# Kernel optimization log

Measured on AMD Instinct MI355X. Metric: run time of the kernel, lower is better.

Reference implementation:

```python
import jax, jax.numpy as jnp
import numpy as np

N_SRC0, N_DST0 = 100000, 20000   # block0: 100k src -> 20k dst
N_DST1 = 4096                    # block1: 20k src -> 4096 dst (seed nodes)


def setup_inputs() -> dict:
    key = jax.random.key(0)
    ks = jax.random.split(key, 8)
    E0, E1 = 640000, 131072
    return {
        "features": jax.random.normal(ks[0], (N_SRC0, 256), jnp.float32),
        "W1": jax.random.normal(ks[1], (256, 256), jnp.float32) * (1.0 / np.sqrt(256)),
        "b1": jnp.zeros((256,), jnp.float32),
        "W2": jax.random.normal(ks[2], (256, 128), jnp.float32) * (1.0 / np.sqrt(256)),
        "b2": jnp.zeros((128,), jnp.float32),
        "src0": jax.random.randint(ks[3], (E0,), 0, N_SRC0, jnp.int32),
        "dst0": jax.random.randint(ks[4], (E0,), 0, N_DST0, jnp.int32),
        "src1": jax.random.randint(ks[5], (E1,), 0, N_DST0, jnp.int32),
        "dst1": jax.random.randint(ks[6], (E1,), 0, N_DST1, jnp.int32),
    }


def _graph_conv(src, dst, n_dst, feat, W, b):
    # DGL GraphConv, norm='both': D_out^{-1/2} gather-sum D_in^{-1/2}, then WX+b.
    n_src = feat.shape[0]
    ones = jnp.ones(src.shape[0], feat.dtype)
    out_deg = jax.ops.segment_sum(ones, src, num_segments=n_src)
    norm_src = jnp.clip(out_deg, 1.0, None) ** -0.5          # [n_src]
    h = feat * norm_src[:, None]
    agg = jax.ops.segment_sum(h[src], dst, num_segments=n_dst)  # sparse SpMM
    in_deg = jax.ops.segment_sum(ones, dst, num_segments=n_dst)
    norm_dst = jnp.clip(in_deg, 1.0, None) ** -0.5           # [n_dst]
    return (agg * norm_dst[:, None]) @ W + b


def reference(features, W1, b1, W2, b2, src0, dst0, src1, dst1):
    x = jax.nn.relu(_graph_conv(src0, dst0, N_DST0, features, W1, b1))
    x = _graph_conv(src1, dst1, N_DST1, x, W2, b2)
    return x
```

## Files before the change

### kernel.cpp

```cpp
#include <hip/hip_runtime.h>
#include <hip/hip_bf16.h>

#define K_DIM 256
#define RSTRIDE 128
#define EPB 8192

#define G0_DB 625
#define G0_SB 256
#define G0_SW 392
#define G0_DCAP 48
#define G0_SCAP 80
#define G1_DB 128
#define G1_SB 64
#define G1_SW 313
#define G1_DCAP 128
#define G1_SCAP 224

typedef short bf16x8 __attribute__((ext_vector_type(8)));
typedef float f32x4 __attribute__((ext_vector_type(4)));

static __device__ __forceinline__ unsigned short f2bf(float x) {
    __hip_bfloat16 b = __float2bfloat16(x);
    return *reinterpret_cast<unsigned short*>(&b);
}
static __device__ __forceinline__ float bflo(unsigned int p) {
    return __uint_as_float(p << 16);
}
static __device__ __forceinline__ float bfhi(unsigned int p) {
    return __uint_as_float(p & 0xffff0000u);
}

template <int NDB, int NSB, int SW, int DCAP, int SCP>
static __device__ __forceinline__ void split_graph_sp(
        const int* __restrict__ src, const int* __restrict__ dst, int E, int chunk,
        int* __restrict__ gdcnt, int* __restrict__ gscnt,
        unsigned int* __restrict__ bdst, unsigned int* __restrict__ bsrc,
        int* sh) {
    const int tid = threadIdx.x;
    const int e0 = chunk * EPB;
    const int n = min(EPB, E - e0);
    for (int i = tid; i < NDB + NSB; i += 256) sh[i] = 0;
    __syncthreads();
    for (int j = tid; j < n; j += 256) {
        int d = dst[e0 + j];
        int s = src[e0 + j];
        int bD = d >> 5;
        int rD = atomicAdd(&sh[bD], 1);
        if (rD < DCAP) bdst[((size_t)chunk * NDB + bD) * DCAP + rD] =
            ((unsigned)s << 5) | (unsigned)(d & 31);
        int bS = (int)((unsigned)s / SW);
        int rS = atomicAdd(&sh[NDB + bS], 1);
        if (rS < SCP) bsrc[((size_t)chunk * NSB + bS) * SCP + rS] = (unsigned)s;
    }
    __syncthreads();
    for (int i = tid; i < NDB; i += 256) gdcnt[chunk * NDB + i] = min(sh[i], DCAP);
    for (int i = tid; i < NSB; i += 256) gscnt[chunk * NSB + i] = min(sh[NDB + i], SCP);
}

__global__ __launch_bounds__(256) void split_mega_kernel(
        const int* __restrict__ src0, const int* __restrict__ dst0, int E0,
        const int* __restrict__ src1, const int* __restrict__ dst1, int E1,
        int* __restrict__ gdcnt0, int* __restrict__ gscnt0,
        unsigned int* __restrict__ bdst0, unsigned int* __restrict__ bsrc0,
        int* __restrict__ gdcnt1, int* __restrict__ gscnt1,
        unsigned int* __restrict__ bdst1, unsigned int* __restrict__ bsrc1,
        int nA0, int nA1,
        const float* __restrict__ feat, unsigned short* __restrict__ h, int total_f,
        int castBlocks,
        const float* __restrict__ W1, uint4* __restrict__ pw1,
        const float* __restrict__ W2, uint4* __restrict__ pw2) {
    __shared__ int sh[G0_DB + G0_SB];
    const int b = blockIdx.x;
    if (b < nA0) {
        split_graph_sp<G0_DB, G0_SB, G0_SW, G0_DCAP, G0_SCAP>(
            src0, dst0, E0, b, gdcnt0, gscnt0, bdst0, bsrc0, sh);
    } else if (b < nA0 + nA1) {
        split_graph_sp<G1_DB, G1_SB, G1_SW, G1_DCAP, G1_SCAP>(
            src1, dst1, E1, b - nA0, gdcnt1, gscnt1, bdst1, bsrc1, sh);
    } else if (b < nA0 + nA1 + castBlocks) {
        int idx = ((b - nA0 - nA1) * blockDim.x + threadIdx.x) * 8;
        if (idx >= total_f) return;
        const float4 v0 = *reinterpret_cast<const float4*>(feat + idx);
        const float4 v1 = *reinterpret_cast<const float4*>(feat + idx + 4);
        union { ushort4 u4[2]; uint4 u; } o;
        o.u4[0].x = f2bf(v0.x); o.u4[0].y = f2bf(v0.y);
        o.u4[0].z = f2bf(v0.z); o.u4[0].w = f2bf(v0.w);
        o.u4[1].x = f2bf(v1.x); o.u4[1].y = f2bf(v1.y);
        o.u4[1].z = f2bf(v1.z); o.u4[1].w = f2bf(v1.w);
        *reinterpret_cast<uint4*>(h + idx) = o.u;
    } else if (b < nA0 + nA1 + castBlocks + 32) {
        int idx = (b - nA0 - nA1 - castBlocks) * blockDim.x + threadIdx.x;
        int lane = idx & 63;
        int kt = (idx >> 6) & 7;
        int nt = idx >> 9;
        int n = nt * 16 + (lane & 15);
        int k = kt * 32 + (lane >> 4) * 8;
        union { unsigned short us[8]; uint4 u; } o;
#pragma unroll
        for (int j = 0; j < 8; ++j) o.us[j] = f2bf(W1[(size_t)(k + j) * 256 + n]);
        pw1[idx] = o.u;
    } else {
        int idx = (b - nA0 - nA1 - castBlocks - 32) * blockDim.x + threadIdx.x;
        int lane = idx & 63;
        int kt = (idx >> 6) & 7;
        int nt = idx >> 9;
        int n = nt * 16 + (lane & 15);
        int k = kt * 32 + (lane >> 4) * 8;
        union { unsigned short us[8]; uint4 u; } o;
#pragma unroll
        for (int j = 0; j < 8; ++j) o.us[j] = f2bf(W2[(size_t)(k + j) * 128 + n]);
        pw2[idx] = o.u;
    }
}

__global__ __launch_bounds__(256) void finalize_kernel(
        int nA0, int nA1,
        const unsigned int* __restrict__ bdst0, const int* __restrict__ gdcnt0,
        int* __restrict__ cnt0, int* __restrict__ esrc0,
        const unsigned int* __restrict__ bdst1, const int* __restrict__ gdcnt1,
        int* __restrict__ cnt1, int* __restrict__ esrc1,
        const unsigned int* __restrict__ bsrc0, const int* __restrict__ gscnt0,
        int* __restrict__ od0,
        const unsigned int* __restrict__ bsrc1, const int* __restrict__ gscnt1,
        int* __restrict__ od1) {
    __shared__ int sh[G0_SW];
    const int tid = threadIdx.x;
    int b = blockIdx.x;
    if (b < G0_DB + G1_DB) {
        const bool g0 = b < G0_DB;
        if (!g0) b -= G0_DB;
        const unsigned int* __restrict__ bd = g0 ? bdst0 : bdst1;
        const int* __restrict__ gc = g0 ? gdcnt0 : gdcnt1;
        const int NDB = g0 ? G0_DB : G1_DB;
        const int DCAP = g0 ? G0_DCAP : G1_DCAP;
        const int nblk = g0 ? nA0 : nA1;
        int* __restrict__ esrc = g0 ? esrc0 : esrc1;
        int* __restrict__ cnt = g0 ? cnt0 : cnt1;
        if (tid < 32) sh[tid] = 0;
        __syncthreads();
        for (int rr = (tid >> 2); rr < nblk; rr += 64) {
            const int c = gc[rr * NDB + b];
            const unsigned int* __restrict__ seg = bd + ((size_t)rr * NDB + b) * DCAP;
            for (int j = (tid & 3); j < c; j += 4) {
                unsigned v = seg[j];
                int dloc = v & 31;
                int s = (int)(v >> 5);
                int slot = atomicAdd(&sh[dloc], 1);
                if (slot < RSTRIDE) esrc[((size_t)(b * 32 + dloc) << 7) + slot] = s;
            }
        }
        __syncthreads();
        if (tid < 32) cnt[b * 32 + tid] = sh[tid];
    } else {
        b -= G0_DB + G1_DB;
        const bool g0 = b < G0_SB;
        if (!g0) b -= G0_SB;
        const unsigned int* __restrict__ bs = g0 ? bsrc0 : bsrc1;
        const int* __restrict__ gc = g0 ? gscnt0 : gscnt1;
        const int NSB = g0 ? G0_SB : G1_SB;
        const int SCP = g0 ? G0_SCAP : G1_SCAP;
        const int SW = g0 ? G0_SW : G1_SW;
        const int NN = g0 ? 100000 : 20000;
        const int nblk = g0 ? nA0 : nA1;
        int* __restrict__ od = g0 ? od0 : od1;
        for (int i = tid; i < SW; i += 256) sh[i] = 0;
        __syncthreads();
        const int base = b * SW;
        for (int rr = (tid >> 2); rr < nblk; rr += 64) {
            const int c = gc[rr * NSB + b];
            const unsigned int* __restrict__ seg = bs + ((size_t)rr * NSB + b) * SCP;
            for (int j = (tid & 3); j < c; j += 4)
                atomicAdd(&sh[(int)seg[j] - base], 1);
        }
        __syncthreads();
        for (int i = tid; i < SW; i += 256) {
            int node = base + i;
            if (node < NN) od[node] = sh[i];
        }
    }
}

template <bool NORM>
static __device__ __forceinline__ void gather4_to_lds(
        const unsigned short* __restrict__ hfeat, const int* __restrict__ esrc,
        const int* __restrict__ cnt, const int* __restrict__ od,
        int m0, int w, int lane, unsigned short (*Alds)[264]) {
#pragma unroll
    for (int k = 0; k < 4; ++k) {
        const int rloc = w * 4 + k;
        const int row = m0 + rloc;
        const int c = cnt[row];
        const int cend = min(c, RSTRIDE);
        const int* __restrict__ ep = esrc + ((size_t)row << 7);
        float a0 = 0.f, a1 = 0.f, a2 = 0.f, a3 = 0.f;
        int i = 0;
        for (; i + 3 < cend; i += 4) {
            int s0 = ep[i];
            int s1 = ep[i + 1];
            int s2 = ep[i + 2];
            int s3 = ep[i + 3];
            float n0 = NORM ? rsqrtf((float)max(od[s0], 1)) : 1.0f;
            float n1 = NORM ? rsqrtf((float)max(od[s1], 1)) : 1.0f;
            float n2 = NORM ? rsqrtf((float)max(od[s2], 1)) : 1.0f;
            float n3 = NORM ? rsqrtf((float)max(od[s3], 1)) : 1.0f;
            const uint2 p0 = *reinterpret_cast<const uint2*>(hfeat + (((size_t)s0) << 8) + lane * 4);
            const uint2 p1 = *reinterpret_cast<const uint2*>(hfeat + (((size_t)s1) << 8) + lane * 4);
            const uint2 p2 = *reinterpret_cast<const uint2*>(hfeat + (((size_t)s2) << 8) + lane * 4);
            const uint2 p3 = *reinterpret_cast<const uint2*>(hfeat + (((size_t)s3) << 8) + lane * 4);
            if (NORM) {
                a0 = fmaf(bflo(p0.x), n0, a0); a1 = fmaf(bfhi(p0.x), n0, a1);
                a2 = fmaf(bflo(p0.y), n0, a2); a3 = fmaf(bfhi(p0.y), n0, a3);
                a0 = fmaf(bflo(p1.x), n1, a0); a1 = fmaf(bfhi(p1.x), n1, a1);
                a2 = fmaf(bflo(p1.y), n1, a2); a3 = fmaf(bfhi(p1.y), n1, a3);
                a0 = fmaf(bflo(p2.x), n2, a0); a1 = fmaf(bfhi(p2.x), n2, a1);
                a2 = fmaf(bflo(p2.y), n2, a2); a3 = fmaf(bfhi(p2.y), n2, a3);
                a0 = fmaf(bflo(p3.x), n3, a0); a1 = fmaf(bfhi(p3.x), n3, a1);
                a2 = fmaf(bflo(p3.y), n3, a2); a3 = fmaf(bfhi(p3.y), n3, a3);
            } else {
                a0 += (bflo(p0.x) + bflo(p1.x)) + (bflo(p2.x) + bflo(p3.x));
                a1 += (bfhi(p0.x) + bfhi(p1.x)) + (bfhi(p2.x) + bfhi(p3.x));
                a2 += (bflo(p0.y) + bflo(p1.y)) + (bflo(p2.y) + bflo(p3.y));
                a3 += (bfhi(p0.y) + bfhi(p1.y)) + (bfhi(p2.y) + bfhi(p3.y));
            }
        }
        for (; i < cend; ++i) {
            int s0 = ep[i];
            float n0 = NORM ? rsqrtf((float)max(od[s0], 1)) : 1.0f;
            const uint2 p0 = *reinterpret_cast<const uint2*>(hfeat + (((size_t)s0) << 8) + lane * 4);
            if (NORM) {
                a0 = fmaf(bflo(p0.x), n0, a0); a1 = fmaf(bfhi(p0.x), n0, a1);
                a2 = fmaf(bflo(p0.y), n0, a2); a3 = fmaf(bfhi(p0.y), n0, a3);
            } else {
                a0 += bflo(p0.x);
                a1 += bfhi(p0.x);
                a2 += bflo(p0.y);
                a3 += bfhi(p0.y);
            }
        }
        float nd = rsqrtf((float)max(c, 1));
        ushort4 o;
        o.x = f2bf(a0 * nd);
        o.y = f2bf(a1 * nd);
        o.z = f2bf(a2 * nd);
        o.w = f2bf(a3 * nd);
        *reinterpret_cast<ushort4*>(&Alds[rloc][lane * 4]) = o;
    }
}

__global__ __launch_bounds__(256) void fused0_kernel(
        const unsigned short* __restrict__ hfeat, const int* __restrict__ esrc,
        const int* __restrict__ cnt, const int* __restrict__ od0,
        const uint4* __restrict__ pW, const float* __restrict__ bias,
        const int* __restrict__ od1, unsigned short* __restrict__ out) {
    __shared__ unsigned short Alds[16][264];
    const int m0 = blockIdx.x * 16;
    const int w = threadIdx.x >> 6;
    const int lane = threadIdx.x & 63;
    gather4_to_lds<true>(hfeat, esrc, cnt, od0, m0, w, lane, Alds);
    __syncthreads();

    bf16x8 a[8];
    const unsigned short* ap = &Alds[lane & 15][(lane >> 4) * 8];
#pragma unroll
    for (int kt = 0; kt < 8; ++kt)
        a[kt] = *reinterpret_cast<const bf16x8*>(ap + kt * 32);

    const int rbase = m0 + (lane >> 4) * 4;
    float nsv[4];
#pragma unroll
    for (int r = 0; r < 4; ++r) nsv[r] = rsqrtf((float)max(od1[rbase + r], 1));

#pragma unroll
    for (int nt = 0; nt < 4; ++nt) {
        const int n0 = w * 64 + nt * 16;
        f32x4 acc = {0.f, 0.f, 0.f, 0.f};
#pragma unroll
        for (int kt = 0; kt < 8; ++kt) {
            bf16x8 b = *reinterpret_cast<const bf16x8*>(&pW[((size_t)(n0 >> 4) * 8 + kt) * 64 + lane]);
            acc = __builtin_amdgcn_mfma_f32_16x16x32_bf16(a[kt], b, acc, 0, 0, 0);
        }
        const int col = n0 + (lane & 15);
        const float bv = bias[col];
#pragma unroll
        for (int r = 0; r < 4; ++r) {
            float v = fmaxf(acc[r] + bv, 0.0f) * nsv[r];
            out[(size_t)(rbase + r) * K_DIM + col] = f2bf(v);
        }
    }
}

__global__ __launch_bounds__(256) void fused1_kernel(
        const unsigned short* __restrict__ xb, const int* __restrict__ esrc,
        const int* __restrict__ cnt,
        const uint4* __restrict__ pW, const float* __restrict__ bias,
        float* __restrict__ out) {
    __shared__ unsigned short Alds[16][264];
    const int m0 = blockIdx.x * 16;
    const int w = threadIdx.x >> 6;
    const int lane = threadIdx.x & 63;
    gather4_to_lds<false>(xb, esrc, cnt, nullptr, m0, w, lane, Alds);
    __syncthreads();

    bf16x8 a[8];
    const unsigned short* ap = &Alds[lane & 15][(lane >> 4) * 8];
#pragma unroll
    for (int kt = 0; kt < 8; ++kt)
        a[kt] = *reinterpret_cast<const bf16x8*>(ap + kt * 32);

    const int rbase = m0 + (lane >> 4) * 4;
#pragma unroll
    for (int nt = 0; nt < 2; ++nt) {
        const int n0 = w * 32 + nt * 16;
        f32x4 acc = {0.f, 0.f, 0.f, 0.f};
#pragma unroll
        for (int kt = 0; kt < 8; ++kt) {
            bf16x8 b = *reinterpret_cast<const bf16x8*>(&pW[((size_t)(n0 >> 4) * 8 + kt) * 64 + lane]);
            acc = __builtin_amdgcn_mfma_f32_16x16x32_bf16(a[kt], b, acc, 0, 0, 0);
        }
        const int col = n0 + (lane & 15);
        const float bv = bias[col];
#pragma unroll
        for (int r = 0; r < 4; ++r)
            out[(size_t)(rbase + r) * 128 + col] = acc[r] + bv;
    }
}

__global__ __launch_bounds__(256) void gatherf_kernel(
        const float* __restrict__ feat, const int* __restrict__ esrc,
        const int* __restrict__ cnt, const int* __restrict__ od,
        float* __restrict__ outbuf, int n_dst) {
    int row = blockIdx.x * (blockDim.x >> 6) + (threadIdx.x >> 6);
    int lane = threadIdx.x & 63;
    if (row >= n_dst) return;
    const int c = cnt[row];
    const int cend = min(c, RSTRIDE);
    const int* __restrict__ ep = esrc + ((size_t)row << 7);
    float4 acc = {0.f, 0.f, 0.f, 0.f};
    for (int i = 0; i < cend; ++i) {
        int s0 = ep[i];
        float n0 = rsqrtf((float)max(od[s0], 1));
        const float4 v0 = *reinterpret_cast<const float4*>(feat + (((size_t)s0) << 8) + lane * 4);
        acc.x = fmaf(v0.x, n0, acc.x); acc.y = fmaf(v0.y, n0, acc.y);
        acc.z = fmaf(v0.z, n0, acc.z); acc.w = fmaf(v0.w, n0, acc.w);
    }
    float nd = rsqrtf((float)max(c, 1));
    float4 o = {acc.x * nd, acc.y * nd, acc.z * nd, acc.w * nd};
    *reinterpret_cast<float4*>(outbuf + (((size_t)row) << 8) + lane * 4) = o;
}

__global__ void edges_kernel(const int* __restrict__ src0, const int* __restrict__ dst0,
                             int* __restrict__ od0, int* __restrict__ cnt0,
                             int* __restrict__ esrc0, int E0,
                             const int* __restrict__ src1, const int* __restrict__ dst1,
                             int* __restrict__ od1, int* __restrict__ cnt1,
                             int* __restrict__ esrc1, int E1) {
    int i = blockIdx.x * blockDim.x + threadIdx.x;
    if (i < E0) {
        int s = src0[i];
        int d = dst0[i];
        atomicAdd(&od0[s], 1);
        int slot = atomicAdd(&cnt0[d], 1);
        if (slot < RSTRIDE) esrc0[(d << 7) + slot] = s;
    } else if (i < E0 + E1) {
        int e = i - E0;
        int s = src1[e];
        int d = dst1[e];
        atomicAdd(&od1[s], 1);
        int slot = atomicAdd(&cnt1[d], 1);
        if (slot < RSTRIDE) esrc1[(d << 7) + slot] = s;
    }
}

template <int ROWS, int NCOLS, bool RELU>
__global__ __launch_bounds__(NCOLS) void gemm_kernel(
        const float* __restrict__ A, const float* __restrict__ W,
        const float* __restrict__ bias, float* __restrict__ out, int M) {
    const int row0 = blockIdx.x * ROWS;
    const int c = threadIdx.x;
    const float* __restrict__ Ablk = A + (size_t)row0 * K_DIM;
    const float* __restrict__ Wc = W + c;

    float acc[ROWS];
#pragma unroll
    for (int r = 0; r < ROWS; ++r) acc[r] = 0.0f;

    float w0 = Wc[0];
    float w1 = Wc[NCOLS];
    float w2 = Wc[2 * NCOLS];
    float w3 = Wc[3 * NCOLS];

#pragma unroll 2
    for (int k = 0; k < K_DIM - 4; k += 4) {
        const float* p = Wc + (size_t)(k + 4) * NCOLS;
        float n0 = p[0];
        float n1 = p[NCOLS];
        float n2 = p[2 * NCOLS];
        float n3 = p[3 * NCOLS];
#pragma unroll
        for (int r = 0; r < ROWS; ++r) {
            const float4 a = *reinterpret_cast<const float4*>(Ablk + r * K_DIM + k);
            acc[r] = fmaf(a.x, w0, acc[r]);
            acc[r] = fmaf(a.y, w1, acc[r]);
            acc[r] = fmaf(a.z, w2, acc[r]);
            acc[r] = fmaf(a.w, w3, acc[r]);
        }
        w0 = n0; w1 = n1; w2 = n2; w3 = n3;
    }
    {
        const int k = K_DIM - 4;
#pragma unroll
        for (int r = 0; r < ROWS; ++r) {
            const float4 a = *reinterpret_cast<const float4*>(Ablk + r * K_DIM + k);
            acc[r] = fmaf(a.x, w0, acc[r]);
            acc[r] = fmaf(a.y, w1, acc[r]);
            acc[r] = fmaf(a.z, w2, acc[r]);
            acc[r] = fmaf(a.w, w3, acc[r]);
        }
    }

    const float b = bias[c];
#pragma unroll
    for (int r = 0; r < ROWS; ++r) {
        float v = acc[r] + b;
        if (RELU) v = fmaxf(v, 0.0f);
        out[(size_t)(row0 + r) * NCOLS + c] = v;
    }
}

extern "C" void kernel_launch(void* const* d_in, const int* in_sizes, int n_in,
                              void* d_out, int out_size, void* d_ws, size_t ws_size,
                              hipStream_t stream) {
    const float* features = (const float*)d_in[0];
    const float* W1 = (const float*)d_in[1];
    const float* b1 = (const float*)d_in[2];
    const float* W2 = (const float*)d_in[3];
    const float* b2 = (const float*)d_in[4];
    const int* src0 = (const int*)d_in[5];
    const int* dst0 = (const int*)d_in[6];
    const int* src1 = (const int*)d_in[7];
    const int* dst1 = (const int*)d_in[8];
    const int E0 = in_sizes[5];
    const int E1 = in_sizes[7];
    const int NSRC0 = 100000, NDST0 = 20000, NDST1 = 4096;
    const int nA0 = (E0 + EPB - 1) / EPB;
    const int nA1 = (E1 + EPB - 1) / EPB;

    char* ws = (char*)d_ws;
    size_t off = 0;
    auto carve = [&](size_t bytes) -> void* {
        void* p = ws + off;
        off = (off + bytes + 255) & ~(size_t)255;
        return p;
    };
    int* od0  = (int*)carve((size_t)NSRC0 * 4);
    int* od1  = (int*)carve((size_t)NDST0 * 4);
    int* cnt0 = (int*)carve((size_t)NDST0 * 4);
    int* cnt1 = (int*)carve((size_t)NDST1 * 4);
    const size_t zero_span = off;
    int* esrc0p = (int*)carve((size_t)NDST0 * RSTRIDE * 4);
    int* esrc1p = (int*)carve((size_t)NDST1 * RSTRIDE * 4);
    uint4* pW1  = (uint4*)carve((size_t)8192 * 16);
    uint4* pW2  = (uint4*)carve((size_t)4096 * 16);
    int* gdcnt0 = (int*)carve((size_t)nA0 * G0_DB * 4);
    int* gscnt0 = (int*)carve((size_t)nA0 * G0_SB * 4);
    int* gdcnt1 = (int*)carve((size_t)nA1 * G1_DB * 4);
    int* gscnt1 = (int*)carve((size_t)nA1 * G1_SB * 4);
    unsigned int* bdst0 = (unsigned int*)carve((size_t)nA0 * G0_DB * G0_DCAP * 4);
    unsigned int* bsrc0 = (unsigned int*)carve((size_t)nA0 * G0_SB * G0_SCAP * 4);
    unsigned int* bdst1 = (unsigned int*)carve((size_t)nA1 * G1_DB * G1_DCAP * 4);
    unsigned int* bsrc1 = (unsigned int*)carve((size_t)nA1 * G1_SB * G1_SCAP * 4);
    const size_t region_span = (size_t)((ws + off) - (char*)bdst0);
    const size_t xbufb_bytes = (size_t)NDST0 * K_DIM * 2;
    unsigned short* xbufb = (region_span >= xbufb_bytes)
        ? (unsigned short*)bdst0
        : (unsigned short*)carve(xbufb_bytes);
    const size_t hfeat_bytes = (size_t)NSRC0 * K_DIM * 2;
    unsigned short* hfeat = (unsigned short*)carve(hfeat_bytes);
    const size_t need_bf16 = off;
    (void)n_in; (void)out_size;

    if (ws_size >= need_bf16) {
        const int total_f = NSRC0 * K_DIM;
        const int castBlocks = (total_f / 8 + 255) / 256;
        split_mega_kernel<<<nA0 + nA1 + castBlocks + 48, 256, 0, stream>>>(
            src0, dst0, E0, src1, dst1, E1,
            gdcnt0, gscnt0, bdst0, bsrc0,
            gdcnt1, gscnt1, bdst1, bsrc1,
            nA0, nA1, features, hfeat, total_f, castBlocks,
            W1, pW1, W2, pW2);
        finalize_kernel<<<G0_DB + G1_DB + G0_SB + G1_SB, 256, 0, stream>>>(
            nA0, nA1,
            bdst0, gdcnt0, cnt0, esrc0p,
            bdst1, gdcnt1, cnt1, esrc1p,
            bsrc0, gscnt0, od0,
            bsrc1, gscnt1, od1);
        fused0_kernel<<<NDST0 / 16, 256, 0, stream>>>(
            hfeat, esrc0p, cnt0, od0, pW1, b1, od1, xbufb);
        fused1_kernel<<<NDST1 / 16, 256, 0, stream>>>(
            xbufb, esrc1p, cnt1, pW2, b2, (float*)d_out);
    } else {
        hipMemsetAsync(ws, 0, zero_span, stream);
        float* agg0 = (float*)carve((size_t)NDST0 * K_DIM * 4);
        float* xbuf = (float*)carve((size_t)NDST0 * K_DIM * 4);
        float* agg1 = (float*)carve((size_t)NDST1 * K_DIM * 4);
        edges_kernel<<<(E0 + E1 + 255) / 256, 256, 0, stream>>>(
            src0, dst0, od0, cnt0, esrc0p, E0,
            src1, dst1, od1, cnt1, esrc1p, E1);
        gatherf_kernel<<<(NDST0 + 3) / 4, 256, 0, stream>>>(features, esrc0p, cnt0, od0,
                                                            agg0, NDST0);
        gemm_kernel<16, 256, true><<<NDST0 / 16, 256, 0, stream>>>(agg0, W1, b1, xbuf, NDST0);
        gatherf_kernel<<<(NDST1 + 3) / 4, 256, 0, stream>>>(xbuf, esrc1p, cnt1, od1,
                                                            agg1, NDST1);
        gemm_kernel<4, 128, false><<<NDST1 / 4, 128, 0, stream>>>(agg1, W2, b2,
                                                                  (float*)d_out, NDST1);
    }
}
```

Baseline: 318.2 us.

## Replace capped bucket scatter with per-chunk counting sort and LDS-tiled finalize

The split phase now does a two-pass counting sort per edge chunk in shared memory (histogram, block exclusive scan, scatter), writing compact sorted segments plus per-bucket offsets instead of fixed-capacity padded buckets that silently dropped overflow. Finalize reads these contiguous segments with per-graph thread-group widths and builds each 32-row esrc tile in LDS before writing it out coalesced. The gather loop is also unrolled to 8 edges with all loads issued before the FMAs to raise memory-level parallelism. This costs extra passes over the edge arrays, a large LDS footprint in the split kernel, and a separate xbufb allocation instead of aliasing.

```diff
diff --git a/kernel.cpp b/kernel.cpp
--- a/kernel.cpp
+++ b/kernel.cpp
@@ -8,13 +8,11 @@
 #define G0_DB 625
 #define G0_SB 256
 #define G0_SW 392
-#define G0_DCAP 48
-#define G0_SCAP 80
 #define G1_DB 128
 #define G1_SB 64
 #define G1_SW 313
-#define G1_DCAP 128
-#define G1_SCAP 224
+
+#define NB_FIN (G0_DB + G1_DB + G0_SB + G1_SB)
 
 typedef short bf16x8 __attribute__((ext_vector_type(8)));
 typedef float f32x4 __attribute__((ext_vector_type(4)));
@@ -30,53 +28,116 @@
     return __uint_as_float(p & 0xffff0000u);
 }
 
-template <int NDB, int NSB, int SW, int DCAP, int SCP>
-static __device__ __forceinline__ void split_graph_sp(
+static __device__ __forceinline__ void block_exscan(
+        const int* __restrict__ hist, int* __restrict__ offs, int* __restrict__ tmp, int M) {
+    const int tid = threadIdx.x;
+    const int S = (M + 255) >> 8;
+    const int base = tid * S;
+    int sum = 0;
+    for (int k = 0; k < S; ++k) {
+        int idx = base + k;
+        if (idx < M) sum += hist[idx];
+    }
+    tmp[tid] = sum;
+    __syncthreads();
+    for (int d = 1; d < 256; d <<= 1) {
+        int v = tmp[tid];
+        int u = (tid >= d) ? tmp[tid - d] : 0;
+        __syncthreads();
+        tmp[tid] = v + u;
+        __syncthreads();
+    }
+    int run = (tid == 0) ? 0 : tmp[tid - 1];
+    for (int k = 0; k < S; ++k) {
+        int idx = base + k;
+        if (idx < M) { offs[idx] = run; run += hist[idx]; }
+    }
+    __syncthreads();
+}
+
+struct SplitSh {
+    int hist[640];
+    int offs[640];
+    int tmp[256];
+    unsigned sorted[EPB];
+};
+
+template <int NDB, int NSB, int SW>
+static __device__ __forceinline__ void split_sort(
         const int* __restrict__ src, const int* __restrict__ dst, int E, int chunk,
-        int* __restrict__ gdcnt, int* __restrict__ gscnt,
-        unsigned int* __restrict__ bdst, unsigned int* __restrict__ bsrc,
-        int* sh) {
+        int* __restrict__ cntD, int* __restrict__ offD,
+        int* __restrict__ cntS, int* __restrict__ offS,
+        unsigned* __restrict__ sortD, unsigned* __restrict__ sortS, SplitSh& sh) {
     const int tid = threadIdx.x;
     const int e0 = chunk * EPB;
     const int n = min(EPB, E - e0);
-    for (int i = tid; i < NDB + NSB; i += 256) sh[i] = 0;
+    for (int i = tid; i < NDB; i += 256) sh.hist[i] = 0;
+    __syncthreads();
+    for (int j = tid; j < n; j += 256) atomicAdd(&sh.hist[dst[e0 + j] >> 5], 1);
+    __syncthreads();
+    block_exscan(sh.hist, sh.offs, sh.tmp, NDB);
+    for (int i = tid; i < NDB; i += 256) {
+        cntD[chunk * NDB + i] = sh.hist[i];
+        offD[chunk * NDB + i] = sh.offs[i];
+    }
     __syncthreads();
     for (int j = tid; j < n; j += 256) {
         int d = dst[e0 + j];
         int s = src[e0 + j];
-        int bD = d >> 5;
-        int rD = atomicAdd(&sh[bD], 1);
-        if (rD < DCAP) bdst[((size_t)chunk * NDB + bD) * DCAP + rD] =
-            ((unsigned)s << 5) | (unsigned)(d & 31);
-        int bS = (int)((unsigned)s / SW);
-        int rS = atomicAdd(&sh[NDB + bS], 1);
-        if (rS < SCP) bsrc[((size_t)chunk * NSB + bS) * SCP + rS] = (unsigned)s;
-    }
-    __syncthreads();
-    for (int i = tid; i < NDB; i += 256) gdcnt[chunk * NDB + i] = min(sh[i], DCAP);
-    for (int i = tid; i < NSB; i += 256) gscnt[chunk * NSB + i] = min(sh[NDB + i], SCP);
-}
-
-__global__ __launch_bounds__(256) void split_mega_kernel(
+        int pos = atomicAdd(&sh.offs[d >> 5], 1);
+        sh.sorted[pos] = ((unsigned)s << 5) | (unsigned)(d & 31);
+    }
+    __syncthreads();
+    {
+        unsigned* __restrict__ gout = sortD + (size_t)chunk * EPB;
+        for (int j = tid; j < n; j += 256) gout[j] = sh.sorted[j];
+    }
+    __syncthreads();
+    for (int i = tid; i < NSB; i += 256) sh.hist[i] = 0;
+    __syncthreads();
+    for (int j = tid; j < n; j += 256)
+        atomicAdd(&sh.hist[(int)((unsigned)src[e0 + j] / SW)], 1);
+    __syncthreads();
+    block_exscan(sh.hist, sh.offs, sh.tmp, NSB);
+    for (int i = tid; i < NSB; i += 256) {
+        cntS[chunk * NSB + i] = sh.hist[i];
+        offS[chunk * NSB + i] = sh.offs[i];
+    }
+    __syncthreads();
+    for (int j = tid; j < n; j += 256) {
+        unsigned s = (unsigned)src[e0 + j];
+        int pos = atomicAdd(&sh.offs[s / SW], 1);
+        sh.sorted[pos] = s;
+    }
+    __syncthreads();
+    {
+        unsigned* __restrict__ gout = sortS + (size_t)chunk * EPB;
+        for (int j = tid; j < n; j += 256) gout[j] = sh.sorted[j];
+    }
+}
+
+__global__ __launch_bounds__(256) void splitA_kernel(
         const int* __restrict__ src0, const int* __restrict__ dst0, int E0,
         const int* __restrict__ src1, const int* __restrict__ dst1, int E1,
-        int* __restrict__ gdcnt0, int* __restrict__ gscnt0,
-        unsigned int* __restrict__ bdst0, unsigned int* __restrict__ bsrc0,
-        int* __restrict__ gdcnt1, int* __restrict__ gscnt1,
-        unsigned int* __restrict__ bdst1, unsigned int* __restrict__ bsrc1,
+        int* __restrict__ cntD0, int* __restrict__ offD0,
+        int* __restrict__ cntS0, int* __restrict__ offS0,
+        unsigned* __restrict__ sortD0, unsigned* __restrict__ sortS0,
+        int* __restrict__ cntD1, int* __restrict__ offD1,
+        int* __restrict__ cntS1, int* __restrict__ offS1,
+        unsigned* __restrict__ sortD1, unsigned* __restrict__ sortS1,
         int nA0, int nA1,
         const float* __restrict__ feat, unsigned short* __restrict__ h, int total_f,
         int castBlocks,
         const float* __restrict__ W1, uint4* __restrict__ pw1,
         const float* __restrict__ W2, uint4* __restrict__ pw2) {
-    __shared__ int sh[G0_DB + G0_SB];
+    __shared__ SplitSh sh;
     const int b = blockIdx.x;
     if (b < nA0) {
-        split_graph_sp<G0_DB, G0_SB, G0_SW, G0_DCAP, G0_SCAP>(
-            src0, dst0, E0, b, gdcnt0, gscnt0, bdst0, bsrc0, sh);
+        split_sort<G0_DB, G0_SB, G0_SW>(src0, dst0, E0, b,
+                                        cntD0, offD0, cntS0, offS0, sortD0, sortS0, sh);
     } else if (b < nA0 + nA1) {
-        split_graph_sp<G1_DB, G1_SB, G1_SW, G1_DCAP, G1_SCAP>(
-            src1, dst1, E1, b - nA0, gdcnt1, gscnt1, bdst1, bsrc1, sh);
+        split_sort<G1_DB, G1_SB, G1_SW>(src1, dst1, E1, b - nA0,
+                                        cntD1, offD1, cntS1, offS1, sortD1, sortS1, sh);
     } else if (b < nA0 + nA1 + castBlocks) {
         int idx = ((b - nA0 - nA1) * blockDim.x + threadIdx.x) * 8;
         if (idx >= total_f) return;
@@ -113,70 +174,81 @@
     }
 }
 
+template <int NDB, int GT>
+static __device__ __forceinline__ void fin_dst(
+        const unsigned* __restrict__ sortD, const int* __restrict__ cntD,
+        const int* __restrict__ offD, int nblk, int b,
+        int* __restrict__ esrc, int* __restrict__ cnt, int* tile, int* rowc) {
+    const int tid = threadIdx.x;
+    if (tid < 32) rowc[tid] = 0;
+    __syncthreads();
+    for (int rr = tid / GT; rr < nblk; rr += 256 / GT) {
+        const int c = cntD[rr * NDB + b];
+        const int o = offD[rr * NDB + b];
+        const unsigned* __restrict__ seg = sortD + (size_t)rr * EPB + o;
+        for (int j = tid % GT; j < c; j += GT) {
+            unsigned v = seg[j];
+            int dloc = v & 31;
+            int s = (int)(v >> 5);
+            int slot = atomicAdd(&rowc[dloc], 1);
+            if (slot < RSTRIDE) tile[(dloc << 7) + slot] = s;
+        }
+    }
+    __syncthreads();
+    int* __restrict__ gout = esrc + ((size_t)b << 12);
+    for (int i = tid; i < 32 * RSTRIDE; i += 256) gout[i] = tile[i];
+    if (tid < 32) cnt[b * 32 + tid] = rowc[tid];
+}
+
+template <int NSB, int SW, int GT>
+static __device__ __forceinline__ void fin_src(
+        const unsigned* __restrict__ sortS, const int* __restrict__ cntS,
+        const int* __restrict__ offS, int nblk, int b, int NN,
+        int* __restrict__ od, int* hist) {
+    const int tid = threadIdx.x;
+    for (int i = tid; i < SW; i += 256) hist[i] = 0;
+    __syncthreads();
+    const int base = b * SW;
+    for (int rr = tid / GT; rr < nblk; rr += 256 / GT) {
+        const int c = cntS[rr * NSB + b];
+        const int o = offS[rr * NSB + b];
+        const unsigned* __restrict__ seg = sortS + (size_t)rr * EPB + o;
+        for (int j = tid % GT; j < c; j += GT)
+            atomicAdd(&hist[(int)seg[j] - base], 1);
+    }
+    __syncthreads();
+    for (int i = tid; i < SW; i += 256) {
+        int node = base + i;
+        if (node < NN) od[node] = hist[i];
+    }
+}
+
 __global__ __launch_bounds__(256) void finalize_kernel(
         int nA0, int nA1,
-        const unsigned int* __restrict__ bdst0, const int* __restrict__ gdcnt0,
-        int* __restrict__ cnt0, int* __restrict__ esrc0,
-        const unsigned int* __restrict__ bdst1, const int* __restrict__ gdcnt1,
-        int* __restrict__ cnt1, int* __restrict__ esrc1,
-        const unsigned int* __restrict__ bsrc0, const int* __restrict__ gscnt0,
-        int* __restrict__ od0,
-        const unsigned int* __restrict__ bsrc1, const int* __restrict__ gscnt1,
-        int* __restrict__ od1) {
-    __shared__ int sh[G0_SW];
-    const int tid = threadIdx.x;
+        const unsigned* __restrict__ sortD0, const int* __restrict__ cntD0,
+        const int* __restrict__ offD0, int* __restrict__ cnt0, int* __restrict__ esrc0,
+        const unsigned* __restrict__ sortD1, const int* __restrict__ cntD1,
+        const int* __restrict__ offD1, int* __restrict__ cnt1, int* __restrict__ esrc1,
+        const unsigned* __restrict__ sortS0, const int* __restrict__ cntS0,
+        const int* __restrict__ offS0, int* __restrict__ od0,
+        const unsigned* __restrict__ sortS1, const int* __restrict__ cntS1,
+        const int* __restrict__ offS1, int* __restrict__ od1) {
+    __shared__ union {
+        struct { int tile[32 * RSTRIDE]; int rowc[32]; } d;
+        int hist[G0_SW];
+    } sh;
     int b = blockIdx.x;
-    if (b < G0_DB + G1_DB) {
-        const bool g0 = b < G0_DB;
-        if (!g0) b -= G0_DB;
-        const unsigned int* __restrict__ bd = g0 ? bdst0 : bdst1;
-        const int* __restrict__ gc = g0 ? gdcnt0 : gdcnt1;
-        const int NDB = g0 ? G0_DB : G1_DB;
-        const int DCAP = g0 ? G0_DCAP : G1_DCAP;
-        const int nblk = g0 ? nA0 : nA1;
-        int* __restrict__ esrc = g0 ? esrc0 : esrc1;
-        int* __restrict__ cnt = g0 ? cnt0 : cnt1;
-        if (tid < 32) sh[tid] = 0;
-        __syncthreads();
-        for (int rr = (tid >> 2); rr < nblk; rr += 64) {
-            const int c = gc[rr * NDB + b];
-            const unsigned int* __restrict__ seg = bd + ((size_t)rr * NDB + b) * DCAP;
-            for (int j = (tid & 3); j < c; j += 4) {
-                unsigned v = seg[j];
-                int dloc = v & 31;
-                int s = (int)(v >> 5);
-                int slot = atomicAdd(&sh[dloc], 1);
-                if (slot < RSTRIDE) esrc[((size_t)(b * 32 + dloc) << 7) + slot] = s;
-            }
-        }
-        __syncthreads();
-        if (tid < 32) cnt[b * 32 + tid] = sh[tid];
+    if (b < G0_DB) {
+        fin_dst<G0_DB, 2>(sortD0, cntD0, offD0, nA0, b, esrc0, cnt0, sh.d.tile, sh.d.rowc);
+    } else if (b < G0_DB + G1_DB) {
+        fin_dst<G1_DB, 16>(sortD1, cntD1, offD1, nA1, b - G0_DB, esrc1, cnt1,
+                           sh.d.tile, sh.d.rowc);
+    } else if (b < G0_DB + G1_DB + G0_SB) {
+        fin_src<G0_SB, G0_SW, 2>(sortS0, cntS0, offS0, nA0, b - G0_DB - G1_DB,
+                                 100000, od0, sh.hist);
     } else {
-        b -= G0_DB + G1_DB;
-        const bool g0 = b < G0_SB;
-        if (!g0) b -= G0_SB;
-        const unsigned int* __restrict__ bs = g0 ? bsrc0 : bsrc1;
-        const int* __restrict__ gc = g0 ? gscnt0 : gscnt1;
-        const int NSB = g0 ? G0_SB : G1_SB;
-        const int SCP = g0 ? G0_SCAP : G1_SCAP;
-        const int SW = g0 ? G0_SW : G1_SW;
-        const int NN = g0 ? 100000 : 20000;
-        const int nblk = g0 ? nA0 : nA1;
-        int* __restrict__ od = g0 ? od0 : od1;
-        for (int i = tid; i < SW; i += 256) sh[i] = 0;
-        __syncthreads();
-        const int base = b * SW;
-        for (int rr = (tid >> 2); rr < nblk; rr += 64) {
-            const int c = gc[rr * NSB + b];
-            const unsigned int* __restrict__ seg = bs + ((size_t)rr * NSB + b) * SCP;
-            for (int j = (tid & 3); j < c; j += 4)
-                atomicAdd(&sh[(int)seg[j] - base], 1);
-        }
-        __syncthreads();
-        for (int i = tid; i < SW; i += 256) {
-            int node = base + i;
-            if (node < NN) od[node] = sh[i];
-        }
+        fin_src<G1_SB, G1_SW, 16>(sortS1, cntS1, offS1, nA1, b - G0_DB - G1_DB - G0_SB,
+                                  20000, od1, sh.hist);
     }
 }
 
@@ -194,33 +266,27 @@
         const int* __restrict__ ep = esrc + ((size_t)row << 7);
         float a0 = 0.f, a1 = 0.f, a2 = 0.f, a3 = 0.f;
         int i = 0;
-        for (; i + 3 < cend; i += 4) {
-            int s0 = ep[i];
-            int s1 = ep[i + 1];
-            int s2 = ep[i + 2];
-            int s3 = ep[i + 3];
-            float n0 = NORM ? rsqrtf((float)max(od[s0], 1)) : 1.0f;
-            float n1 = NORM ? rsqrtf((float)max(od[s1], 1)) : 1.0f;
-            float n2 = NORM ? rsqrtf((float)max(od[s2], 1)) : 1.0f;
-            float n3 = NORM ? rsqrtf((float)max(od[s3], 1)) : 1.0f;
-            const uint2 p0 = *reinterpret_cast<const uint2*>(hfeat + (((size_t)s0) << 8) + lane * 4);
-            const uint2 p1 = *reinterpret_cast<const uint2*>(hfeat + (((size_t)s1) << 8) + lane * 4);
-            const uint2 p2 = *reinterpret_cast<const uint2*>(hfeat + (((size_t)s2) << 8) + lane * 4);
-            const uint2 p3 = *reinterpret_cast<const uint2*>(hfeat + (((size_t)s3) << 8) + lane * 4);
-            if (NORM) {
-                a0 = fmaf(bflo(p0.x), n0, a0); a1 = fmaf(bfhi(p0.x), n0, a1);
-                a2 = fmaf(bflo(p0.y), n0, a2); a3 = fmaf(bfhi(p0.y), n0, a3);
-                a0 = fmaf(bflo(p1.x), n1, a0); a1 = fmaf(bfhi(p1.x), n1, a1);
-                a2 = fmaf(bflo(p1.y), n1, a2); a3 = fmaf(bfhi(p1.y), n1, a3);
-                a0 = fmaf(bflo(p2.x), n2, a0); a1 = fmaf(bfhi(p2.x), n2, a1);
-                a2 = fmaf(bflo(p2.y), n2, a2); a3 = fmaf(bfhi(p2.y), n2, a3);
-                a0 = fmaf(bflo(p3.x), n3, a0); a1 = fmaf(bfhi(p3.x), n3, a1);
-                a2 = fmaf(bflo(p3.y), n3, a2); a3 = fmaf(bfhi(p3.y), n3, a3);
-            } else {
-                a0 += (bflo(p0.x) + bflo(p1.x)) + (bflo(p2.x) + bflo(p3.x));
-                a1 += (bfhi(p0.x) + bfhi(p1.x)) + (bfhi(p2.x) + bfhi(p3.x));
-                a2 += (bflo(p0.y) + bflo(p1.y)) + (bflo(p2.y) + bflo(p3.y));
-                a3 += (bfhi(p0.y) + bfhi(p1.y)) + (bfhi(p2.y) + bfhi(p3.y));
+        for (; i + 7 < cend; i += 8) {
+            int s[8];
+            uint2 p[8];
+            float nn[8];
+#pragma unroll
+            for (int u = 0; u < 8; ++u) s[u] = ep[i + u];
+#pragma unroll
+            for (int u = 0; u < 8; ++u)
+                p[u] = *reinterpret_cast<const uint2*>(hfeat + (((size_t)s[u]) << 8) + lane * 4);
+#pragma unroll
+            for (int u = 0; u < 8; ++u)
+                nn[u] = NORM ? rsqrtf((float)max(od[s[u]], 1)) : 1.0f;
+#pragma unroll
+            for (int u = 0; u < 8; ++u) {
+                if (NORM) {
+                    a0 = fmaf(bflo(p[u].x), nn[u], a0); a1 = fmaf(bfhi(p[u].x), nn[u], a1);
+                    a2 = fmaf(bflo(p[u].y), nn[u], a2); a3 = fmaf(bfhi(p[u].y), nn[u], a3);
+                } else {
+                    a0 += bflo(p[u].x); a1 += bfhi(p[u].x);
+                    a2 += bflo(p[u].y); a3 += bfhi(p[u].y);
+                }
             }
         }
         for (; i < cend; ++i) {
@@ -231,10 +297,8 @@
                 a0 = fmaf(bflo(p0.x), n0, a0); a1 = fmaf(bfhi(p0.x), n0, a1);
                 a2 = fmaf(bflo(p0.y), n0, a2); a3 = fmaf(bfhi(p0.y), n0, a3);
             } else {
-                a0 += bflo(p0.x);
-                a1 += bfhi(p0.x);
-                a2 += bflo(p0.y);
-                a3 += bfhi(p0.y);
+                a0 += bflo(p0.x); a1 += bfhi(p0.x);
+                a2 += bflo(p0.y); a3 += bfhi(p0.y);
             }
         }
         float nd = rsqrtf((float)max(c, 1));
@@ -461,39 +525,38 @@
     int* esrc1p = (int*)carve((size_t)NDST1 * RSTRIDE * 4);
     uint4* pW1  = (uint4*)carve((size_t)8192 * 16);
     uint4* pW2  = (uint4*)carve((size_t)4096 * 16);
-    int* gdcnt0 = (int*)carve((size_t)nA0 * G0_DB * 4);
-    int* gscnt0 = (int*)carve((size_t)nA0 * G0_SB * 4);
-    int* gdcnt1 = (int*)carve((size_t)nA1 * G1_DB * 4);
-    int* gscnt1 = (int*)carve((size_t)nA1 * G1_SB * 4);
-    unsigned int* bdst0 = (unsigned int*)carve((size_t)nA0 * G0_DB * G0_DCAP * 4);
-    unsigned int* bsrc0 = (unsigned int*)carve((size_t)nA0 * G0_SB * G0_SCAP * 4);
-    unsigned int* bdst1 = (unsigned int*)carve((size_t)nA1 * G1_DB * G1_DCAP * 4);
-    unsigned int* bsrc1 = (unsigned int*)carve((size_t)nA1 * G1_SB * G1_SCAP * 4);
-    const size_t region_span = (size_t)((ws + off) - (char*)bdst0);
-    const size_t xbufb_bytes = (size_t)NDST0 * K_DIM * 2;
-    unsigned short* xbufb = (region_span >= xbufb_bytes)
-        ? (unsigned short*)bdst0
-        : (unsigned short*)carve(xbufb_bytes);
-    const size_t hfeat_bytes = (size_t)NSRC0 * K_DIM * 2;
-    unsigned short* hfeat = (unsigned short*)carve(hfeat_bytes);
+    int* cntD0 = (int*)carve((size_t)nA0 * G0_DB * 4);
+    int* offD0 = (int*)carve((size_t)nA0 * G0_DB * 4);
+    int* cntS0 = (int*)carve((size_t)nA0 * G0_SB * 4);
+    int* offS0 = (int*)carve((size_t)nA0 * G0_SB * 4);
+    int* cntD1 = (int*)carve((size_t)nA1 * G1_DB * 4);
+    int* offD1 = (int*)carve((size_t)nA1 * G1_DB * 4);
+    int* cntS1 = (int*)carve((size_t)nA1 * G1_SB * 4);
+    int* offS1 = (int*)carve((size_t)nA1 * G1_SB * 4);
+    unsigned* sortD0 = (unsigned*)carve((size_t)nA0 * EPB * 4);
+    unsigned* sortS0 = (unsigned*)carve((size_t)nA0 * EPB * 4);
+    unsigned* sortD1 = (unsigned*)carve((size_t)nA1 * EPB * 4);
+    unsigned* sortS1 = (unsigned*)carve((size_t)nA1 * EPB * 4);
+    unsigned short* xbufb = (unsigned short*)carve((size_t)NDST0 * K_DIM * 2);
+    unsigned short* hfeat = (unsigned short*)carve((size_t)NSRC0 * K_DIM * 2);
     const size_t need_bf16 = off;
     (void)n_in; (void)out_size;
 
     if (ws_size >= need_bf16) {
         const int total_f = NSRC0 * K_DIM;
         const int castBlocks = (total_f / 8 + 255) / 256;
-        split_mega_kernel<<<nA0 + nA1 + castBlocks + 48, 256, 0, stream>>>(
+        splitA_kernel<<<nA0 + nA1 + castBlocks + 48, 256, 0, stream>>>(
             src0, dst0, E0, src1, dst1, E1,
-            gdcnt0, gscnt0, bdst0, bsrc0,
-            gdcnt1, gscnt1, bdst1, bsrc1,
+            cntD0, offD0, cntS0, offS0, sortD0, sortS0,
+            cntD1, offD1, cntS1, offS1, sortD1, sortS1,
             nA0, nA1, features, hfeat, total_f, castBlocks,
             W1, pW1, W2, pW2);
-        finalize_kernel<<<G0_DB + G1_DB + G0_SB + G1_SB, 256, 0, stream>>>(
+        finalize_kernel<<<NB_FIN, 256, 0, stream>>>(
             nA0, nA1,
-            bdst0, gdcnt0, cnt0, esrc0p,
-            bdst1, gdcnt1, cnt1, esrc1p,
-            bsrc0, gscnt0, od0,
-            bsrc1, gscnt1, od1);
+            sortD0, cntD0, offD0, cnt0, esrc0p,
+            sortD1, cntD1, offD1, cnt1, esrc1p,
+            sortS0, cntS0, offS0, od0,
+            sortS1, cntS1, offS1, od1);
         fused0_kernel<<<NDST0 / 16, 256, 0, stream>>>(
             hfeat, esrc0p, cnt0, od0, pW1, b1, od1, xbufb);
         fused1_kernel<<<NDST1 / 16, 256, 0, stream>>>(
```

Result: faster. 296.3 us (-6.9%).
